# Performance work log

Measured on AMD Instinct MI355X. Metric: run time of the kernel, lower is better.

Reference implementation:

```python
import jax, jax.numpy as jnp
import numpy as np

B, T, A, H = 128, 256, 8, 1024

def setup_inputs() -> dict:
    key = jax.random.key(0)
    ks = jax.random.split(key, 8)
    s = 0.05
    return {
        "actions": jax.random.normal(ks[0], (B, T, A), jnp.float32),
        "hidden_state": jax.random.normal(ks[1], (B, H), jnp.float32),
        "fc_w": jax.random.normal(ks[2], (H, A), jnp.float32) * s,
        "fc_b": jax.random.normal(ks[3], (H,), jnp.float32) * s,
        "w_ih": jax.random.normal(ks[4], (3 * H, H), jnp.float32) * s,
        "w_hh": jax.random.normal(ks[5], (3 * H, H), jnp.float32) * s,
        "b_ih": jax.random.normal(ks[6], (3 * H,), jnp.float32) * s,
        "b_hh": jax.random.normal(ks[7], (3 * H,), jnp.float32) * s,
    }

def reference(actions, hidden_state, fc_w, fc_b, w_ih, w_hh, b_ih, b_hh):
    # Linear + ReLU input projection: [B,T,A] -> [B,T,H]
    x = jax.nn.relu(jnp.einsum('bta,ha->bth', actions, fc_w) + fc_b)
    # Precompute input-side gate projections for all timesteps: [B,T,3H]
    xp = jnp.einsum('bth,gh->btg', x, w_ih) + b_ih

    def step(h, xt):
        hp = h @ w_hh.T + b_hh                       # [B,3H]
        xr, xz, xn = jnp.split(xt, 3, axis=-1)       # PyTorch gate order: r, z, n
        hr, hz, hn = jnp.split(hp, 3, axis=-1)
        r = jax.nn.sigmoid(xr + hr)
        z = jax.nn.sigmoid(xz + hz)
        n = jnp.tanh(xn + r * hn)
        h_new = (1.0 - z) * n + z * h
        return h_new, h_new

    _, ys = jax.lax.scan(step, hidden_state, jnp.swapaxes(xp, 0, 1))  # ys: [T,B,H]
    return jnp.swapaxes(ys, 0, 1)                    # [B,T,H]
```

## Files before the change

kernel.cpp:

```cpp
#include <hip/hip_runtime.h>

typedef __attribute__((ext_vector_type(8))) short short8;
typedef __attribute__((ext_vector_type(4))) float f32x4;

#define NB 128
#define NT 256
#define NA 8
#define NH 1024
#define NG 3072

__device__ __forceinline__ unsigned short f2bf(float f) {
    unsigned v;
    __builtin_memcpy(&v, &f, 4);
    v = v + 0x7fffu + ((v >> 16) & 1u);
    return (unsigned short)(v >> 16);
}
__device__ __forceinline__ float sigm_f(float u)  { return 1.f / (1.f + __expf(-u)); }
__device__ __forceinline__ float tanh_f(float u)  { return 1.f - 2.f / (1.f + __expf(2.f * u)); }


__global__ __launch_bounds__(256) void wconv_kernel(
    const float* __restrict__ src, unsigned short* __restrict__ dst, int n)
{
    for (int i = (blockIdx.x * 256 + threadIdx.x) * 4; i < n; i += gridDim.x * 256 * 4) {
        float4 v = *(const float4*)(src + i);
        ushort4 o;
        o.x = f2bf(v.x); o.y = f2bf(v.y); o.z = f2bf(v.z); o.w = f2bf(v.w);
        *(ushort4*)(dst + i) = o;
    }
}

__global__ __launch_bounds__(256) void xproj_bf16_kernel(
    const float* __restrict__ actions,
    const float* __restrict__ fc_w,
    const float* __restrict__ fc_b,
    unsigned short* __restrict__ xbf)
{
    const int bt  = blockIdx.x;
    const int tid = threadIdx.x;

    const float* ap = actions + (size_t)bt * NA;
    float a[8];
#pragma unroll
    for (int i = 0; i < 8; ++i) a[i] = ap[i];

    const int h0 = tid * 4;
    unsigned short r[4];
#pragma unroll
    for (int j = 0; j < 4; ++j) {
        const float* wp = fc_w + (size_t)(h0 + j) * NA;
        float acc = fc_b[h0 + j];
#pragma unroll
        for (int i = 0; i < 8; ++i) acc += a[i] * wp[i];
        r[j] = f2bf(fmaxf(acc, 0.f));
    }
    ushort4 pk;
    pk.x = r[0]; pk.y = r[1]; pk.z = r[2]; pk.w = r[3];
    *(ushort4*)(xbf + (size_t)bt * NH + h0) = pk;
}



__device__ __forceinline__ void bb_barrier(unsigned* cnt, unsigned target) {
    __syncthreads();
    if (threadIdx.x == 0) {
        __hip_atomic_fetch_add(cnt, 1u, __ATOMIC_RELAXED, __HIP_MEMORY_SCOPE_AGENT);
        while (__hip_atomic_load(cnt, __ATOMIC_RELAXED, __HIP_MEMORY_SCOPE_AGENT) < target)
            __builtin_amdgcn_s_sleep(1);
    }
    __syncthreads();
    asm volatile("" ::: "memory");
}

__device__ __forceinline__ short8 ld_hB16(const unsigned short* p) {
    union { unsigned long long u[2]; short8 v; } r;
    r.u[0] = __hip_atomic_load((const unsigned long long*)p,
                               __ATOMIC_RELAXED, __HIP_MEMORY_SCOPE_AGENT);
    r.u[1] = __hip_atomic_load((const unsigned long long*)(p + 4),
                               __ATOMIC_RELAXED, __HIP_MEMORY_SCOPE_AGENT);
    return r.v;
}

__device__ __forceinline__ void st_hB2(unsigned short* p, unsigned short lo, unsigned short hi) {
    unsigned v = (unsigned)lo | ((unsigned)hi << 16);
    __hip_atomic_store((unsigned*)p, v, __ATOMIC_RELAXED, __HIP_MEMORY_SCOPE_AGENT);
}

__global__ __launch_bounds__(256, 1) void gru_persistent(
    float* __restrict__ out,
    const unsigned short* __restrict__ xbf,
    const unsigned short* __restrict__ wih,
    const unsigned short* __restrict__ whh,
    const float* __restrict__ b_ih,
    const float* __restrict__ b_hh,
    const float* __restrict__ hidden0,
    unsigned short* __restrict__ hB,
    unsigned* __restrict__ cntbase)
{
    const int tid = threadIdx.x;
    const int kw = tid >> 6, lane = tid & 63, col = lane & 15, q = lane >> 4;
    const int bb = blockIdx.x >> 6, hc = blockIdx.x & 63;
    const int koff = kw * 256 + q * 8;
    unsigned* cnt = cntbase + bb * 64;

    __shared__ float hp_d[4][32][49];
    __shared__ float xq_d[4][32][49];

    short8 wf_hh[3][8], wf_ih[3][8];
#pragma unroll
    for (int g = 0; g < 3; ++g) {
        const unsigned short* Wh = whh + (size_t)(g * NH + hc * 16 + col) * NH + koff;
        const unsigned short* Wi = wih + (size_t)(g * NH + hc * 16 + col) * NH + koff;
#pragma unroll
        for (int s = 0; s < 8; ++s) {
            wf_hh[g][s] = *(const short8*)(Wh + s * 32);
            wf_ih[g][s] = *(const short8*)(Wi + s * 32);
        }
    }

    const int eb = tid >> 3, eh2 = (tid & 7) * 2, ebg = bb * 32 + eb;
    const int hg0 = hc * 16 + eh2;

    float bi_r[2][3], bh_r[2][3];
#pragma unroll
    for (int e = 0; e < 2; ++e)
#pragma unroll
        for (int g = 0; g < 3; ++g) {
            bi_r[e][g] = b_ih[g * NH + hg0 + e];
            bh_r[e][g] = b_hh[g * NH + hg0 + e];
        }

    const size_t xrow   = (size_t)(bb * 32 + col) * (NT * NH) + koff;
    const size_t xtile1 = (size_t)16 * NT * NH;

    short8 xa0[8], xa1[8];
    {
        const unsigned short* Ax = xbf + xrow;
#pragma unroll
        for (int s = 0; s < 8; ++s) {
            xa0[s] = *(const short8*)(Ax + s * 32);
            xa1[s] = *(const short8*)(Ax + xtile1 + s * 32);
        }
    }

    float xq_r[2][3];
    float hprev[2];

    {
        f32x4 xq[6];
#pragma unroll
        for (int i = 0; i < 6; ++i) xq[i] = (f32x4){0.f, 0.f, 0.f, 0.f};
#pragma unroll
        for (int s = 0; s < 8; ++s) {
            xq[0] = __builtin_amdgcn_mfma_f32_16x16x32_bf16(xa0[s], wf_ih[0][s], xq[0], 0, 0, 0);
            xq[1] = __builtin_amdgcn_mfma_f32_16x16x32_bf16(xa0[s], wf_ih[1][s], xq[1], 0, 0, 0);
            xq[2] = __builtin_amdgcn_mfma_f32_16x16x32_bf16(xa0[s], wf_ih[2][s], xq[2], 0, 0, 0);
            xq[3] = __builtin_amdgcn_mfma_f32_16x16x32_bf16(xa1[s], wf_ih[0][s], xq[3], 0, 0, 0);
            xq[4] = __builtin_amdgcn_mfma_f32_16x16x32_bf16(xa1[s], wf_ih[1][s], xq[4], 0, 0, 0);
            xq[5] = __builtin_amdgcn_mfma_f32_16x16x32_bf16(xa1[s], wf_ih[2][s], xq[5], 0, 0, 0);
        }
#pragma unroll
        for (int m = 0; m < 2; ++m)
#pragma unroll
            for (int n = 0; n < 3; ++n)
#pragma unroll
                for (int i = 0; i < 4; ++i)
                    xq_d[kw][m * 16 + q * 4 + i][n * 16 + col] = xq[m * 3 + n][i];
        __syncthreads();
#pragma unroll
        for (int e = 0; e < 2; ++e) {
            const int hl = eh2 + e;
            float s0 = 0.f, s1 = 0.f, s2 = 0.f;
#pragma unroll
            for (int c = 0; c < 4; ++c) {
                s0 += xq_d[c][eb][hl];
                s1 += xq_d[c][eb][16 + hl];
                s2 += xq_d[c][eb][32 + hl];
            }
            xq_r[e][0] = s0; xq_r[e][1] = s1; xq_r[e][2] = s2;
        }
        float2 h0 = *(const float2*)(hidden0 + (size_t)ebg * NH + hg0);
        hprev[0] = h0.x; hprev[1] = h0.y;
        st_hB2(hB + (size_t)ebg * NH + hg0, f2bf(h0.x), f2bf(h0.y));
    }
    {
        const unsigned short* Ax = xbf + (size_t)1 * NH + xrow;
#pragma unroll
        for (int s = 0; s < 8; ++s) {
            xa0[s] = *(const short8*)(Ax + s * 32);
            xa1[s] = *(const short8*)(Ax + xtile1 + s * 32);
        }
    }
    bb_barrier(cnt, 64u);

    for (int t = 0; t < NT; ++t) {
        f32x4 hp[6];
#pragma unroll
        for (int i = 0; i < 6; ++i) hp[i] = (f32x4){0.f, 0.f, 0.f, 0.f};
        const unsigned short* Ah = hB + (size_t)(t & 1) * (NB * NH)
                                      + (size_t)(bb * 32 + col) * NH + koff;
#pragma unroll
        for (int s = 0; s < 8; ++s) {
            short8 a0 = ld_hB16(Ah + s * 32);
            short8 a1 = ld_hB16(Ah + 16 * NH + s * 32);
            hp[0] = __builtin_amdgcn_mfma_f32_16x16x32_bf16(a0, wf_hh[0][s], hp[0], 0, 0, 0);
            hp[1] = __builtin_amdgcn_mfma_f32_16x16x32_bf16(a0, wf_hh[1][s], hp[1], 0, 0, 0);
            hp[2] = __builtin_amdgcn_mfma_f32_16x16x32_bf16(a0, wf_hh[2][s], hp[2], 0, 0, 0);
            hp[3] = __builtin_amdgcn_mfma_f32_16x16x32_bf16(a1, wf_hh[0][s], hp[3], 0, 0, 0);
            hp[4] = __builtin_amdgcn_mfma_f32_16x16x32_bf16(a1, wf_hh[1][s], hp[4], 0, 0, 0);
            hp[5] = __builtin_amdgcn_mfma_f32_16x16x32_bf16(a1, wf_hh[2][s], hp[5], 0, 0, 0);
        }

        f32x4 xq[6];
#pragma unroll
        for (int i = 0; i < 6; ++i) xq[i] = (f32x4){0.f, 0.f, 0.f, 0.f};
        if (t + 1 < NT) {
#pragma unroll
            for (int s = 0; s < 8; ++s) {
                xq[0] = __builtin_amdgcn_mfma_f32_16x16x32_bf16(xa0[s], wf_ih[0][s], xq[0], 0, 0, 0);
                xq[1] = __builtin_amdgcn_mfma_f32_16x16x32_bf16(xa0[s], wf_ih[1][s], xq[1], 0, 0, 0);
                xq[2] = __builtin_amdgcn_mfma_f32_16x16x32_bf16(xa0[s], wf_ih[2][s], xq[2], 0, 0, 0);
                xq[3] = __builtin_amdgcn_mfma_f32_16x16x32_bf16(xa1[s], wf_ih[0][s], xq[3], 0, 0, 0);
                xq[4] = __builtin_amdgcn_mfma_f32_16x16x32_bf16(xa1[s], wf_ih[1][s], xq[4], 0, 0, 0);
                xq[5] = __builtin_amdgcn_mfma_f32_16x16x32_bf16(xa1[s], wf_ih[2][s], xq[5], 0, 0, 0);
            }
        }

#pragma unroll
        for (int m = 0; m < 2; ++m)
#pragma unroll
            for (int n = 0; n < 3; ++n)
#pragma unroll
                for (int i = 0; i < 4; ++i) {
                    hp_d[kw][m * 16 + q * 4 + i][n * 16 + col] = hp[m * 3 + n][i];
                    xq_d[kw][m * 16 + q * 4 + i][n * 16 + col] = xq[m * 3 + n][i];
                }
        __syncthreads();

        float hn2[2];
#pragma unroll
        for (int e = 0; e < 2; ++e) {
            const int hl = eh2 + e;
            float hr = bh_r[e][0], hz = bh_r[e][1], hn = bh_r[e][2];
#pragma unroll
            for (int c = 0; c < 4; ++c) {
                hr += hp_d[c][eb][hl];
                hz += hp_d[c][eb][16 + hl];
                hn += hp_d[c][eb][32 + hl];
            }
            const float r  = sigm_f(xq_r[e][0] + bi_r[e][0] + hr);
            const float z  = sigm_f(xq_r[e][1] + bi_r[e][1] + hz);
            const float nn = tanh_f(xq_r[e][2] + bi_r[e][2] + r * hn);
            const float hv = (1.f - z) * nn + z * hprev[e];
            hprev[e] = hv;
            hn2[e] = hv;
            float s0 = 0.f, s1 = 0.f, s2 = 0.f;
#pragma unroll
            for (int c = 0; c < 4; ++c) {
                s0 += xq_d[c][eb][hl];
                s1 += xq_d[c][eb][16 + hl];
                s2 += xq_d[c][eb][32 + hl];
            }
            xq_r[e][0] = s0; xq_r[e][1] = s1; xq_r[e][2] = s2;
        }
        float2 o2; o2.x = hn2[0]; o2.y = hn2[1];
        *(float2*)(out + ((size_t)ebg * NT + t) * NH + hg0) = o2;
        st_hB2(hB + (size_t)((t + 1) & 1) * (NB * NH) + (size_t)ebg * NH + hg0,
               f2bf(hn2[0]), f2bf(hn2[1]));

        if (t + 2 < NT) {
            const unsigned short* Ax = xbf + (size_t)(t + 2) * NH + xrow;
#pragma unroll
            for (int s = 0; s < 8; ++s) {
                xa0[s] = *(const short8*)(Ax + s * 32);
                xa1[s] = *(const short8*)(Ax + xtile1 + s * 32);
            }
        }

        bb_barrier(cnt, (unsigned)(t + 2) * 64u);
    }
}

__global__ __launch_bounds__(256) void zero_cnt_kernel(unsigned* __restrict__ c)
{
    c[threadIdx.x] = 0u;
}


__device__ __forceinline__ void xq_gemm(
    const unsigned short* xslice, const unsigned short* w_ih,
    int bb, int hc, int col, int koff, f32x4 acc[6])
{
    const unsigned short* Ax = xslice + (size_t)(bb * 32 + col) * (NT * NH) + koff;
    const size_t tile1 = (size_t)16 * NT * NH;
    const unsigned short* W0 = w_ih + (size_t)(0 * NH + hc * 16 + col) * NH + koff;
    const unsigned short* W1 = w_ih + (size_t)(1 * NH + hc * 16 + col) * NH + koff;
    const unsigned short* W2 = w_ih + (size_t)(2 * NH + hc * 16 + col) * NH + koff;
#pragma unroll
    for (int s = 0; s < 8; ++s) {
        short8 a0 = *(const short8*)(Ax + s * 32);
        short8 a1 = *(const short8*)(Ax + tile1 + s * 32);
        short8 b0 = *(const short8*)(W0 + s * 32);
        short8 b1 = *(const short8*)(W1 + s * 32);
        short8 b2 = *(const short8*)(W2 + s * 32);
        acc[0] = __builtin_amdgcn_mfma_f32_16x16x32_bf16(a0, b0, acc[0], 0, 0, 0);
        acc[1] = __builtin_amdgcn_mfma_f32_16x16x32_bf16(a0, b1, acc[1], 0, 0, 0);
        acc[2] = __builtin_amdgcn_mfma_f32_16x16x32_bf16(a0, b2, acc[2], 0, 0, 0);
        acc[3] = __builtin_amdgcn_mfma_f32_16x16x32_bf16(a1, b0, acc[3], 0, 0, 0);
        acc[4] = __builtin_amdgcn_mfma_f32_16x16x32_bf16(a1, b1, acc[4], 0, 0, 0);
        acc[5] = __builtin_amdgcn_mfma_f32_16x16x32_bf16(a1, b2, acc[5], 0, 0, 0);
    }
}

__global__ __launch_bounds__(256) void gru_init_kernel(
    const unsigned short* __restrict__ xbf,
    const float* __restrict__ hidden0,
    const unsigned short* __restrict__ w_ih,
    float* __restrict__ xp, float* __restrict__ hF, unsigned short* __restrict__ hB)
{
    const int tid = threadIdx.x;
    const int kw = tid >> 6, lane = tid & 63, col = lane & 15, q = lane >> 4;
    const int bb = blockIdx.x >> 6, hc = blockIdx.x & 63;
    const int koff = kw * 256 + q * 8;

    __shared__ float xq_d[4][32][49];

    f32x4 acc[6];
#pragma unroll
    for (int i = 0; i < 6; ++i) acc[i] = (f32x4){0.f, 0.f, 0.f, 0.f};
    xq_gemm(xbf, w_ih, bb, hc, col, koff, acc);

#pragma unroll
    for (int m = 0; m < 2; ++m)
#pragma unroll
        for (int n = 0; n < 3; ++n)
#pragma unroll
            for (int i = 0; i < 4; ++i)
                xq_d[kw][m * 16 + q * 4 + i][n * 16 + col] = acc[m * 3 + n][i];
    __syncthreads();

    const int b = tid >> 3, h2 = (tid & 7) * 2, bg = bb * 32 + b;
#pragma unroll
    for (int e = 0; e < 2; ++e) {
        const int hl = h2 + e;
        const int hg = hc * 16 + hl;
        float s0 = 0.f, s1 = 0.f, s2 = 0.f;
#pragma unroll
        for (int c = 0; c < 4; ++c) {
            s0 += xq_d[c][b][hl];
            s1 += xq_d[c][b][16 + hl];
            s2 += xq_d[c][b][32 + hl];
        }
        float* xpd = xp + (size_t)bg * NG;
        xpd[hg]          = s0;
        xpd[NH + hg]     = s1;
        xpd[2 * NH + hg] = s2;
        const float hv = hidden0[(size_t)bg * NH + hg];
        hF[(size_t)bg * NH + hg] = hv;
        hB[(size_t)bg * NH + hg] = f2bf(hv);
    }
}

__global__ __launch_bounds__(256) void gru_step_kernel(
    float* __restrict__ out,
    const unsigned short* __restrict__ xbf,
    const unsigned short* __restrict__ w_ih,
    const unsigned short* __restrict__ w_hh,
    const float* __restrict__ b_ih,
    const float* __restrict__ b_hh,
    float* __restrict__ xp, float* __restrict__ hF, unsigned short* __restrict__ hB,
    int t)
{
    const int tid = threadIdx.x;
    const int kw = tid >> 6, lane = tid & 63, col = lane & 15, q = lane >> 4;
    const int bb = blockIdx.x >> 6, hc = blockIdx.x & 63;
    const int koff = kw * 256 + q * 8;

    __shared__ float hp_d[4][32][49];
    __shared__ float xq_d[4][32][49];

    f32x4 hp[6];
#pragma unroll
    for (int i = 0; i < 6; ++i) hp[i] = (f32x4){0.f, 0.f, 0.f, 0.f};
    {
        const unsigned short* Ah = hB + (size_t)(t & 1) * (NB * NH)
                                      + (size_t)(bb * 32 + col) * NH + koff;
        const unsigned short* W0 = w_hh + (size_t)(0 * NH + hc * 16 + col) * NH + koff;
        const unsigned short* W1 = w_hh + (size_t)(1 * NH + hc * 16 + col) * NH + koff;
        const unsigned short* W2 = w_hh + (size_t)(2 * NH + hc * 16 + col) * NH + koff;
#pragma unroll
        for (int s = 0; s < 8; ++s) {
            short8 a0 = *(const short8*)(Ah + s * 32);
            short8 a1 = *(const short8*)(Ah + 16 * NH + s * 32);
            short8 b0 = *(const short8*)(W0 + s * 32);
            short8 b1 = *(const short8*)(W1 + s * 32);
            short8 b2 = *(const short8*)(W2 + s * 32);
            hp[0] = __builtin_amdgcn_mfma_f32_16x16x32_bf16(a0, b0, hp[0], 0, 0, 0);
            hp[1] = __builtin_amdgcn_mfma_f32_16x16x32_bf16(a0, b1, hp[1], 0, 0, 0);
            hp[2] = __builtin_amdgcn_mfma_f32_16x16x32_bf16(a0, b2, hp[2], 0, 0, 0);
            hp[3] = __builtin_amdgcn_mfma_f32_16x16x32_bf16(a1, b0, hp[3], 0, 0, 0);
            hp[4] = __builtin_amdgcn_mfma_f32_16x16x32_bf16(a1, b1, hp[4], 0, 0, 0);
            hp[5] = __builtin_amdgcn_mfma_f32_16x16x32_bf16(a1, b2, hp[5], 0, 0, 0);
        }
    }

    f32x4 xq[6];
#pragma unroll
    for (int i = 0; i < 6; ++i) xq[i] = (f32x4){0.f, 0.f, 0.f, 0.f};
    if (t + 1 < NT)
        xq_gemm(xbf + (size_t)(t + 1) * NH, w_ih, bb, hc, col, koff, xq);

#pragma unroll
    for (int m = 0; m < 2; ++m)
#pragma unroll
        for (int n = 0; n < 3; ++n)
#pragma unroll
            for (int i = 0; i < 4; ++i) {
                hp_d[kw][m * 16 + q * 4 + i][n * 16 + col] = hp[m * 3 + n][i];
                xq_d[kw][m * 16 + q * 4 + i][n * 16 + col] = xq[m * 3 + n][i];
            }
    __syncthreads();

    const int b = tid >> 3, h2 = (tid & 7) * 2, bg = bb * 32 + b;
#pragma unroll
    for (int e = 0; e < 2; ++e) {
        const int hl = h2 + e;
        const int hg = hc * 16 + hl;

        const float* xps = xp + (size_t)(t & 1) * (NB * NG) + (size_t)bg * NG;
        float xr = xps[hg]          + b_ih[hg];
        float xz = xps[NH + hg]     + b_ih[NH + hg];
        float xn = xps[2 * NH + hg] + b_ih[2 * NH + hg];
        float hr = b_hh[hg];
        float hz = b_hh[NH + hg];
        float hn = b_hh[2 * NH + hg];
#pragma unroll
        for (int c = 0; c < 4; ++c) {
            hr += hp_d[c][b][hl];
            hz += hp_d[c][b][16 + hl];
            hn += hp_d[c][b][32 + hl];
        }
        const float r = sigm_f(xr + hr);
        const float z = sigm_f(xz + hz);
        const float n = tanh_f(xn + r * hn);
        const float hprev = hF[(size_t)(t & 1) * (NB * NH) + (size_t)bg * NH + hg];
        const float hnew  = (1.f - z) * n + z * hprev;

        hF[(size_t)((t + 1) & 1) * (NB * NH) + (size_t)bg * NH + hg] = hnew;
        hB[(size_t)((t + 1) & 1) * (NB * NH) + (size_t)bg * NH + hg] = f2bf(hnew);
        out[((size_t)bg * NT + t) * NH + hg] = hnew;

        if (t + 1 < NT) {
            float s0 = 0.f, s1 = 0.f, s2 = 0.f;
#pragma unroll
            for (int c = 0; c < 4; ++c) {
                s0 += xq_d[c][b][hl];
                s1 += xq_d[c][b][16 + hl];
                s2 += xq_d[c][b][32 + hl];
            }
            float* xpd = xp + (size_t)((t + 1) & 1) * (NB * NG) + (size_t)bg * NG;
            xpd[hg]          = s0;
            xpd[NH + hg]     = s1;
            xpd[2 * NH + hg] = s2;
        }
    }
}


__global__ __launch_bounds__(256) void xproj_f32_kernel(
    const float* __restrict__ actions, const float* __restrict__ fc_w,
    const float* __restrict__ fc_b, float* __restrict__ xbuf)
{
    const int bt = blockIdx.x, tid = threadIdx.x;
    const float* ap = actions + (size_t)bt * NA;
    float a[8];
#pragma unroll
    for (int i = 0; i < 8; ++i) a[i] = ap[i];
    const int h0 = tid * 4;
    float4 r;
    float* rp = &r.x;
#pragma unroll
    for (int j = 0; j < 4; ++j) {
        const float* wp = fc_w + (size_t)(h0 + j) * NA;
        float acc = fc_b[h0 + j];
#pragma unroll
        for (int i = 0; i < 8; ++i) acc += a[i] * wp[i];
        rp[j] = fmaxf(acc, 0.f);
    }
    *(float4*)(xbuf + (size_t)bt * NH + h0) = r;
}

__global__ __launch_bounds__(512) void hinit_kernel(
    const float* __restrict__ hidden0, float* __restrict__ hF)
{
    const int i = blockIdx.x * 512 + threadIdx.x;
    hF[i] = hidden0[i];
}

__global__ __launch_bounds__(512) void gru_step_valu(
    float* xout, const float* __restrict__ w_ih, const float* __restrict__ w_hh,
    const float* __restrict__ b_ih, const float* __restrict__ b_hh,
    float* __restrict__ hF, int t)
{
    const int tid = threadIdx.x;
    const int b = tid >> 4, hl = tid & 15;
    const int bb = blockIdx.x >> 6, hc = blockIdx.x & 63;
    const int bg = bb * 32 + b, hg = hc * 16 + hl;

    const float* hrow = hF + (size_t)(t & 1) * (NB * NH) + (size_t)bg * NH;
    const float* xrow = xout + ((size_t)bg * NT + t) * NH;
    const float* wrh = w_hh + (size_t)(0 * NH + hg) * NH;
    const float* wzh = w_hh + (size_t)(1 * NH + hg) * NH;
    const float* wnh = w_hh + (size_t)(2 * NH + hg) * NH;
    const float* wrx = w_ih + (size_t)(0 * NH + hg) * NH;
    const float* wzx = w_ih + (size_t)(1 * NH + hg) * NH;
    const float* wnx = w_ih + (size_t)(2 * NH + hg) * NH;

    float hr = 0.f, hz = 0.f, hn = 0.f, xr = 0.f, xz = 0.f, xn = 0.f;
#pragma unroll 4
    for (int k = 0; k < NH; k += 4) {
        float4 hv = *(const float4*)(hrow + k);
        float4 xv = *(const float4*)(xrow + k);
        float4 w;
        w = *(const float4*)(wrh + k); hr += hv.x*w.x + hv.y*w.y + hv.z*w.z + hv.w*w.w;
        w = *(const float4*)(wzh + k); hz += hv.x*w.x + hv.y*w.y + hv.z*w.z + hv.w*w.w;
        w = *(const float4*)(wnh + k); hn += hv.x*w.x + hv.y*w.y + hv.z*w.z + hv.w*w.w;
        w = *(const float4*)(wrx + k); xr += xv.x*w.x + xv.y*w.y + xv.z*w.z + xv.w*w.w;
        w = *(const float4*)(wzx + k); xz += xv.x*w.x + xv.y*w.y + xv.z*w.z + xv.w*w.w;
        w = *(const float4*)(wnx + k); xn += xv.x*w.x + xv.y*w.y + xv.z*w.z + xv.w*w.w;
    }
    const float r = sigm_f(xr + b_ih[hg] + hr + b_hh[hg]);
    const float z = sigm_f(xz + b_ih[NH + hg] + hz + b_hh[NH + hg]);
    const float n = tanh_f(xn + b_ih[2 * NH + hg] + r * (hn + b_hh[2 * NH + hg]));
    const float hprev = hrow[hg];
    const float hnew  = (1.f - z) * n + z * hprev;
    hF[(size_t)((t + 1) & 1) * (NB * NH) + (size_t)bg * NH + hg] = hnew;
    if (t > 0)
        xout[((size_t)bg * NT + (t - 1)) * NH + hg] = hprev;
}

__global__ __launch_bounds__(512) void tail_kernel(
    const float* __restrict__ hF, float* __restrict__ xout)
{
    const int i = blockIdx.x * 512 + threadIdx.x;
    const int b = i >> 10, h = i & (NH - 1);
    xout[((size_t)b * NT + (NT - 1)) * NH + h] = hF[i];
}


extern "C" void kernel_launch(void* const* d_in, const int* in_sizes, int n_in,
                              void* d_out, int out_size, void* d_ws, size_t ws_size,
                              hipStream_t stream)
{
    (void)in_sizes; (void)n_in; (void)out_size;

    const float* actions = (const float*)d_in[0];
    const float* hidden  = (const float*)d_in[1];
    const float* fc_w    = (const float*)d_in[2];
    const float* fc_b    = (const float*)d_in[3];
    const float* w_ih    = (const float*)d_in[4];
    const float* w_hh    = (const float*)d_in[5];
    const float* b_ih    = (const float*)d_in[6];
    const float* b_hh    = (const float*)d_in[7];

    float* outp = (float*)d_out;

    const size_t NEED = 84410368;

    if (ws_size >= NEED) {
        unsigned short* wih_bf = (unsigned short*)d_ws;
        unsigned short* whh_bf = (unsigned short*)((char*)d_ws + 6291456);
        unsigned short* xbf    = (unsigned short*)((char*)d_ws + 12582912);
        unsigned*       cnt    = (unsigned*)((char*)d_ws + 79691776);
        float*          xp     = (float*)((char*)d_ws + 79691776);
        float*          hF     = (float*)((char*)d_ws + 82837504);
        unsigned short* hB     = (unsigned short*)((char*)d_ws + 83886080);

        wconv_kernel<<<dim3(3072), dim3(256), 0, stream>>>(w_ih, wih_bf, NG * NH);
        wconv_kernel<<<dim3(3072), dim3(256), 0, stream>>>(w_hh, whh_bf, NG * NH);
        xproj_bf16_kernel<<<dim3(NB * NT), dim3(256), 0, stream>>>(actions, fc_w, fc_b, xbf);
        zero_cnt_kernel<<<dim3(1), dim3(256), 0, stream>>>(cnt);

        void* kargs[] = { (void*)&outp, (void*)&xbf, (void*)&wih_bf, (void*)&whh_bf,
                          (void*)&b_ih, (void*)&b_hh, (void*)&hidden, (void*)&hB,
                          (void*)&cnt };
        hipError_t ce = hipLaunchCooperativeKernel((const void*)gru_persistent,
                                                   dim3(256), dim3(256), kargs, 0, stream);
        if (ce != hipSuccess) {
            gru_init_kernel<<<dim3(256), dim3(256), 0, stream>>>(xbf, hidden, wih_bf, xp, hF, hB);
            for (int t = 0; t < NT; ++t)
                gru_step_kernel<<<dim3(256), dim3(256), 0, stream>>>(outp, xbf, wih_bf, whh_bf,
                                                                     b_ih, b_hh, xp, hF, hB, t);
        }
    } else {
        float* hF = (float*)d_ws;
        xproj_f32_kernel<<<dim3(NB * NT), dim3(256), 0, stream>>>(actions, fc_w, fc_b, outp);
        hinit_kernel<<<dim3(256), dim3(512), 0, stream>>>(hidden, hF);
        for (int t = 0; t < NT; ++t)
            gru_step_valu<<<dim3(256), dim3(512), 0, stream>>>(outp, w_ih, w_hh,
                                                               b_ih, b_hh, hF, t);
        tail_kernel<<<dim3(256), dim3(512), 0, stream>>>(hF, outp);
    }
}
```

Baseline: 2.402 ms.

## Replace counter barrier with per-block epoch flags and reorder step for overlap

The group barrier changes from a single shared atomic counter to per-block epoch slots: each block stores its own epoch and one wavefront polls all 64 slots, which removes contention on one atomic address. Block-to-(batch, hidden-chunk) mapping is permuted so the blocks of a batch group spread across XCDs differently. Within each step the hidden-state loads are issued up front and overlapped with the input-projection MFMAs, and the h state is published and the output written (nontemporal) before the local reduction of the next xq, so other blocks are released sooner. This trades more polling loads per wait for lower barrier latency on the critical path.

```diff
diff --git a/kernel.cpp b/kernel.cpp
--- a/kernel.cpp
+++ b/kernel.cpp
@@ -2,6 +2,7 @@
 
 typedef __attribute__((ext_vector_type(8))) short short8;
 typedef __attribute__((ext_vector_type(4))) float f32x4;
+typedef __attribute__((ext_vector_type(2))) float f32x2;
 
 #define NB 128
 #define NT 256
@@ -61,12 +62,18 @@
 
 
 
-__device__ __forceinline__ void bb_barrier(unsigned* cnt, unsigned target) {
+__device__ __forceinline__ void bb_barrier(unsigned* slots, int mySlot, unsigned epoch) {
     __syncthreads();
-    if (threadIdx.x == 0) {
-        __hip_atomic_fetch_add(cnt, 1u, __ATOMIC_RELAXED, __HIP_MEMORY_SCOPE_AGENT);
-        while (__hip_atomic_load(cnt, __ATOMIC_RELAXED, __HIP_MEMORY_SCOPE_AGENT) < target)
+    if (threadIdx.x < 64) {
+        if (threadIdx.x == 0)
+            __hip_atomic_store(slots + mySlot, epoch,
+                               __ATOMIC_RELAXED, __HIP_MEMORY_SCOPE_AGENT);
+        for (;;) {
+            unsigned v = __hip_atomic_load(slots + (int)threadIdx.x,
+                                           __ATOMIC_RELAXED, __HIP_MEMORY_SCOPE_AGENT);
+            if (__all((int)(v >= epoch))) break;
             __builtin_amdgcn_s_sleep(1);
+        }
     }
     __syncthreads();
     asm volatile("" ::: "memory");
@@ -95,13 +102,15 @@
     const float* __restrict__ b_hh,
     const float* __restrict__ hidden0,
     unsigned short* __restrict__ hB,
-    unsigned* __restrict__ cntbase)
+    unsigned* __restrict__ slotbase)
 {
     const int tid = threadIdx.x;
     const int kw = tid >> 6, lane = tid & 63, col = lane & 15, q = lane >> 4;
-    const int bb = blockIdx.x >> 6, hc = blockIdx.x & 63;
+    const int bid = (int)blockIdx.x;
+    const int bb = (bid & 7) >> 1;
+    const int hc = ((bid >> 3) << 1) | (bid & 1);
     const int koff = kw * 256 + q * 8;
-    unsigned* cnt = cntbase + bb * 64;
+    unsigned* slots = slotbase + bb * 64;
 
     __shared__ float hp_d[4][32][49];
     __shared__ float xq_d[4][32][49];
@@ -191,24 +200,18 @@
             xa1[s] = *(const short8*)(Ax + xtile1 + s * 32);
         }
     }
-    bb_barrier(cnt, 64u);
+    bb_barrier(slots, hc, 1u);
 
     for (int t = 0; t < NT; ++t) {
-        f32x4 hp[6];
-#pragma unroll
-        for (int i = 0; i < 6; ++i) hp[i] = (f32x4){0.f, 0.f, 0.f, 0.f};
-        const unsigned short* Ah = hB + (size_t)(t & 1) * (NB * NH)
-                                      + (size_t)(bb * 32 + col) * NH + koff;
-#pragma unroll
-        for (int s = 0; s < 8; ++s) {
-            short8 a0 = ld_hB16(Ah + s * 32);
-            short8 a1 = ld_hB16(Ah + 16 * NH + s * 32);
-            hp[0] = __builtin_amdgcn_mfma_f32_16x16x32_bf16(a0, wf_hh[0][s], hp[0], 0, 0, 0);
-            hp[1] = __builtin_amdgcn_mfma_f32_16x16x32_bf16(a0, wf_hh[1][s], hp[1], 0, 0, 0);
-            hp[2] = __builtin_amdgcn_mfma_f32_16x16x32_bf16(a0, wf_hh[2][s], hp[2], 0, 0, 0);
-            hp[3] = __builtin_amdgcn_mfma_f32_16x16x32_bf16(a1, wf_hh[0][s], hp[3], 0, 0, 0);
-            hp[4] = __builtin_amdgcn_mfma_f32_16x16x32_bf16(a1, wf_hh[1][s], hp[4], 0, 0, 0);
-            hp[5] = __builtin_amdgcn_mfma_f32_16x16x32_bf16(a1, wf_hh[2][s], hp[5], 0, 0, 0);
+        short8 ha0[8], ha1[8];
+        {
+            const unsigned short* Ah = hB + (size_t)(t & 1) * (NB * NH)
+                                          + (size_t)(bb * 32 + col) * NH + koff;
+#pragma unroll
+            for (int s = 0; s < 8; ++s) {
+                ha0[s] = ld_hB16(Ah + s * 32);
+                ha1[s] = ld_hB16(Ah + 16 * NH + s * 32);
+            }
         }
 
         f32x4 xq[6];
@@ -226,6 +229,19 @@
             }
         }
 
+        f32x4 hp[6];
+#pragma unroll
+        for (int i = 0; i < 6; ++i) hp[i] = (f32x4){0.f, 0.f, 0.f, 0.f};
+#pragma unroll
+        for (int s = 0; s < 8; ++s) {
+            hp[0] = __builtin_amdgcn_mfma_f32_16x16x32_bf16(ha0[s], wf_hh[0][s], hp[0], 0, 0, 0);
+            hp[1] = __builtin_amdgcn_mfma_f32_16x16x32_bf16(ha0[s], wf_hh[1][s], hp[1], 0, 0, 0);
+            hp[2] = __builtin_amdgcn_mfma_f32_16x16x32_bf16(ha0[s], wf_hh[2][s], hp[2], 0, 0, 0);
+            hp[3] = __builtin_amdgcn_mfma_f32_16x16x32_bf16(ha1[s], wf_hh[0][s], hp[3], 0, 0, 0);
+            hp[4] = __builtin_amdgcn_mfma_f32_16x16x32_bf16(ha1[s], wf_hh[1][s], hp[4], 0, 0, 0);
+            hp[5] = __builtin_amdgcn_mfma_f32_16x16x32_bf16(ha1[s], wf_hh[2][s], hp[5], 0, 0, 0);
+        }
+
 #pragma unroll
         for (int m = 0; m < 2; ++m)
 #pragma unroll
@@ -236,6 +252,15 @@
                     xq_d[kw][m * 16 + q * 4 + i][n * 16 + col] = xq[m * 3 + n][i];
                 }
         __syncthreads();
+
+        if (t + 2 < NT) {
+            const unsigned short* Ax = xbf + (size_t)(t + 2) * NH + xrow;
+#pragma unroll
+            for (int s = 0; s < 8; ++s) {
+                xa0[s] = *(const short8*)(Ax + s * 32);
+                xa1[s] = *(const short8*)(Ax + xtile1 + s * 32);
+            }
+        }
 
         float hn2[2];
 #pragma unroll
@@ -254,6 +279,15 @@
             const float hv = (1.f - z) * nn + z * hprev[e];
             hprev[e] = hv;
             hn2[e] = hv;
+        }
+        st_hB2(hB + (size_t)((t + 1) & 1) * (NB * NH) + (size_t)ebg * NH + hg0,
+               f2bf(hn2[0]), f2bf(hn2[1]));
+        f32x2 o2; o2.x = hn2[0]; o2.y = hn2[1];
+        __builtin_nontemporal_store(o2, (f32x2*)(out + ((size_t)ebg * NT + t) * NH + hg0));
+
+#pragma unroll
+        for (int e = 0; e < 2; ++e) {
+            const int hl = eh2 + e;
             float s0 = 0.f, s1 = 0.f, s2 = 0.f;
 #pragma unroll
             for (int c = 0; c < 4; ++c) {
@@ -263,21 +297,8 @@
             }
             xq_r[e][0] = s0; xq_r[e][1] = s1; xq_r[e][2] = s2;
         }
-        float2 o2; o2.x = hn2[0]; o2.y = hn2[1];
-        *(float2*)(out + ((size_t)ebg * NT + t) * NH + hg0) = o2;
-        st_hB2(hB + (size_t)((t + 1) & 1) * (NB * NH) + (size_t)ebg * NH + hg0,
-               f2bf(hn2[0]), f2bf(hn2[1]));
-
-        if (t + 2 < NT) {
-            const unsigned short* Ax = xbf + (size_t)(t + 2) * NH + xrow;
-#pragma unroll
-            for (int s = 0; s < 8; ++s) {
-                xa0[s] = *(const short8*)(Ax + s * 32);
-                xa1[s] = *(const short8*)(Ax + xtile1 + s * 32);
-            }
-        }
-
-        bb_barrier(cnt, (unsigned)(t + 2) * 64u);
+
+        bb_barrier(slots, hc, (unsigned)(t + 2));
     }
 }
 
@@ -571,7 +592,7 @@
         unsigned short* wih_bf = (unsigned short*)d_ws;
         unsigned short* whh_bf = (unsigned short*)((char*)d_ws + 6291456);
         unsigned short* xbf    = (unsigned short*)((char*)d_ws + 12582912);
-        unsigned*       cnt    = (unsigned*)((char*)d_ws + 79691776);
+        unsigned*       slots  = (unsigned*)((char*)d_ws + 79691776);
         float*          xp     = (float*)((char*)d_ws + 79691776);
         float*          hF     = (float*)((char*)d_ws + 82837504);
         unsigned short* hB     = (unsigned short*)((char*)d_ws + 83886080);
@@ -579,11 +600,11 @@
         wconv_kernel<<<dim3(3072), dim3(256), 0, stream>>>(w_ih, wih_bf, NG * NH);
         wconv_kernel<<<dim3(3072), dim3(256), 0, stream>>>(w_hh, whh_bf, NG * NH);
         xproj_bf16_kernel<<<dim3(NB * NT), dim3(256), 0, stream>>>(actions, fc_w, fc_b, xbf);
-        zero_cnt_kernel<<<dim3(1), dim3(256), 0, stream>>>(cnt);
+        zero_cnt_kernel<<<dim3(1), dim3(256), 0, stream>>>(slots);
 
         void* kargs[] = { (void*)&outp, (void*)&xbf, (void*)&wih_bf, (void*)&whh_bf,
                           (void*)&b_ih, (void*)&b_hh, (void*)&hidden, (void*)&hB,
-                          (void*)&cnt };
+                          (void*)&slots };
         hipError_t ce = hipLaunchCooperativeKernel((const void*)gru_persistent,
                                                    dim3(256), dim3(256), kargs, 0, stream);
         if (ce != hipSuccess) {
```

Result: slower. 2.823 ms (+17.5%).
